# Kernel tuning notes

Hardware: AMD Instinct MI355X
Metric: run time of the kernel (lower is better)

Reference implementation:

```python
import jax, jax.numpy as jnp
import numpy as np

N = 100000   # nodes
E = 1600000  # edges
G = 256      # graphs
NF = 7       # node features
EF = 3       # edge features (in/out)
UD = 2       # global feature dim
H = 128      # hidden dim
NL = 2       # MetaLayers = n_layers - 1
DOUT = 1


def _lin_init(k, fan_in, fan_out):
    return jax.random.normal(k, (fan_in, fan_out), jnp.float32) / np.sqrt(fan_in)


def _mlp2(h, W1, b1, W2, b2):
    return jax.nn.relu(h @ W1 + b1) @ W2 + b2


def setup_inputs() -> dict:
    key = jax.random.key(0)
    ks = jax.random.split(key, 40)
    x = jax.random.normal(ks[0], (N, NF), jnp.float32)
    edge_index = jax.random.randint(ks[1], (2, E), 0, N, jnp.int64)
    edge_attr = jax.random.normal(ks[2], (E, EF), jnp.float32)
    u = jax.random.normal(ks[3], (G, UD), jnp.float32)
    batch = jnp.sort(jax.random.randint(ks[4], (N,), 0, G, jnp.int64))
    # stacked per-layer params (NL identical layers)
    e_in = 2 * NF + EF          # 17
    n_in = NF + 3 * EF + UD     # 18
    eW1 = jnp.stack([_lin_init(ks[5 + i], e_in, H) for i in range(NL)])
    eb1 = jnp.zeros((NL, H), jnp.float32)
    eW2 = jnp.stack([_lin_init(ks[7 + i], H, EF) for i in range(NL)])
    eb2 = jnp.zeros((NL, EF), jnp.float32)
    nW1 = jnp.stack([_lin_init(ks[9 + i], n_in, H) for i in range(NL)])
    nb1 = jnp.zeros((NL, H), jnp.float32)
    nW2 = jnp.stack([_lin_init(ks[11 + i], H, NF) for i in range(NL)])
    nb2 = jnp.zeros((NL, NF), jnp.float32)
    # output head: 3*node_out + global_in -> H -> H -> H -> dim_out
    oW1 = _lin_init(ks[20], 3 * NF + UD, H); ob1 = jnp.zeros((H,), jnp.float32)
    oW2 = _lin_init(ks[21], H, H); ob2 = jnp.zeros((H,), jnp.float32)
    oW3 = _lin_init(ks[22], H, H); ob3 = jnp.zeros((H,), jnp.float32)
    oW4 = _lin_init(ks[23], H, DOUT); ob4 = jnp.zeros((DOUT,), jnp.float32)
    return dict(x=x, edge_attr=edge_attr, u=u,
                eW1=eW1, eb1=eb1, eW2=eW2, eb2=eb2,
                nW1=nW1, nb1=nb1, nW2=nW2, nb2=nb2,
                oW1=oW1, ob1=ob1, oW2=oW2, ob2=ob2,
                oW3=oW3, ob3=ob3, oW4=oW4, ob4=ob4,
                edge_index=edge_index, batch=batch)


def _segment_reduce3(vals, seg, num):
    # add / max (empty -> 0, matching torch_scatter fill) / mean
    s = jax.ops.segment_sum(vals, seg, num_segments=num)
    cnt = jax.ops.segment_sum(jnp.ones((vals.shape[0], 1), vals.dtype), seg, num_segments=num)
    m = jax.ops.segment_max(vals, seg, num_segments=num)
    m = jnp.where(cnt > 0, m, jnp.zeros_like(m))
    mean = s / jnp.maximum(cnt, 1.0)
    return s, m, mean, cnt


def reference(x, edge_attr, u, eW1, eb1, eW2, eb2, nW1, nb1, nW2, nb2,
              oW1, ob1, oW2, ob2, oW3, ob3, oW4, ob4, edge_index, batch):
    row, col = edge_index[0], edge_index[1]
    for l in range(NL):
        # EdgeModel: gather src/dest node feats + edge feats -> MLP
        e_in = jnp.concatenate([x[row], x[col], edge_attr], axis=1)  # [E, 2*NF+EF]
        edge_attr = _mlp2(e_in, eW1[l], eb1[l], eW2[l], eb2[l])      # [E, EF]
        # NodeModel: three scatter reductions over incoming edges (col)
        s, m, mean, _ = _segment_reduce3(edge_attr, col, N)
        n_in = jnp.concatenate([x, s, m, mean, u[batch]], axis=1)    # [N, NF+3*EF+UD]
        x = _mlp2(n_in, nW1[l], nb1[l], nW2[l], nb2[l])              # [N, NF]
    # global pools per graph
    s, m, mean, _ = _segment_reduce3(x, batch, G)
    h = jnp.concatenate([s, mean, m, u], axis=1)                     # [G, 3*NF+UD]
    h = jax.nn.relu(h @ oW1 + ob1)
    h = jax.nn.relu(h @ oW2 + ob2)
    h = jax.nn.relu(h @ oW3 + ob3)
    return h @ oW4 + ob4                                             # [G, DOUT]
```

## Files before the change

### kernel.cpp

```cpp
#include <hip/hip_runtime.h>

#define NN 100000
#define NE 1600000
#define NG 256
#define NB 391

typedef __attribute__((ext_vector_type(8))) short short8v;
typedef __attribute__((ext_vector_type(4))) float float4v;

__device__ __forceinline__ unsigned short f2bf(float f) {
    unsigned u = __float_as_uint(f);
    return (unsigned short)((u + 0x7FFFu + ((u >> 16) & 1u)) >> 16);
}

__global__ __launch_bounds__(256) void zero_kernel(float* __restrict__ p, int n) {
    int i = blockIdx.x * 256 + threadIdx.x;
    if (i < n) p[i] = 0.f;
}

__global__ __launch_bounds__(256) void rank_kernel(
    const int* __restrict__ col, unsigned* __restrict__ cnt,
    unsigned* __restrict__ rank) {
    int e = blockIdx.x * 256 + threadIdx.x;
    rank[e] = atomicAdd(&cnt[col[e]], 1u);
}

__global__ __launch_bounds__(256) void gbound_kernel(
    const int* __restrict__ batch, int* __restrict__ gstart) {
    int n = blockIdx.x * 256 + threadIdx.x;
    if (n >= NN) return;
    int b = batch[n];
    int bp = (n == 0) ? -1 : batch[n - 1];
    for (int g = bp + 1; g <= b; ++g) gstart[g] = n;
    if (n == NN - 1) {
        for (int g = b + 1; g <= NG; ++g) gstart[g] = NN;
    }
}

__global__ __launch_bounds__(256) void bsum_kernel(
    const unsigned* __restrict__ cnt, unsigned* __restrict__ bsum) {
    __shared__ unsigned sm[256];
    int i = blockIdx.x * 256 + threadIdx.x;
    sm[threadIdx.x] = (i < NN) ? cnt[i] : 0u;
    __syncthreads();
    for (int s = 128; s > 0; s >>= 1) {
        if (threadIdx.x < s) sm[threadIdx.x] += sm[threadIdx.x + s];
        __syncthreads();
    }
    if (threadIdx.x == 0) bsum[blockIdx.x] = sm[0];
}

__global__ __launch_bounds__(512) void bscan_kernel(
    const unsigned* __restrict__ bsum, unsigned* __restrict__ boff) {
    __shared__ unsigned a[512], b[512];
    int t = threadIdx.x;
    a[t] = (t < NB) ? bsum[t] : 0u;
    __syncthreads();
    unsigned* src = a; unsigned* dst = b;
    for (int off = 1; off < 512; off <<= 1) {
        unsigned v = src[t];
        if (t >= off) v += src[t - off];
        dst[t] = v;
        __syncthreads();
        unsigned* tmp = src; src = dst; dst = tmp;
    }
    if (t < NB) boff[t] = (t == 0) ? 0u : src[t - 1];
}

__global__ __launch_bounds__(256) void start_kernel(
    const unsigned* __restrict__ cnt, const unsigned* __restrict__ boff,
    unsigned* __restrict__ start) {
    __shared__ unsigned a[256], b[256];
    int t = threadIdx.x;
    int i = blockIdx.x * 256 + t;
    unsigned v = (i < NN) ? cnt[i] : 0u;
    a[t] = v;
    __syncthreads();
    unsigned* src = a; unsigned* dst = b;
    for (int off = 1; off < 256; off <<= 1) {
        unsigned x = src[t];
        if (t >= off) x += src[t - off];
        dst[t] = x;
        __syncthreads();
        unsigned* tmp = src; src = dst; dst = tmp;
    }
    unsigned excl = src[t] - v;
    unsigned st = boff[blockIdx.x] + excl;
    if (i < NN) {
        start[i] = st;
        if (i == NN - 1) start[NN] = st + v;
    }
}

__global__ __launch_bounds__(256) void scatter_kernel(
    const int* __restrict__ row, const int* __restrict__ col,
    const float* __restrict__ ea,
    const unsigned* __restrict__ start, const unsigned* __restrict__ rank,
    int2* __restrict__ rc, float* __restrict__ eab) {
    int e = blockIdx.x * 256 + threadIdx.x;
    int c = col[e];
    unsigned t = start[c] + rank[e];
    rc[t] = make_int2(row[e], c);
    eab[(size_t)t * 3 + 0] = ea[(size_t)e * 3 + 0];
    eab[(size_t)t * 3 + 1] = ea[(size_t)e * 3 + 1];
    eab[(size_t)t * 3 + 2] = ea[(size_t)e * 3 + 2];
}

__global__ __launch_bounds__(256) void prep_kernel(
    const float* __restrict__ eW1, const float* __restrict__ eb1, const float* __restrict__ eW2,
    const float* __restrict__ nW1, const float* __restrict__ nb1, const float* __restrict__ nW2,
    short* __restrict__ ewf, float* __restrict__ w2f, float* __restrict__ b1f,
    float* __restrict__ nwt)
{
    int t = blockIdx.x * 256 + threadIdx.x;
    const int EWF = 2 * 4096;
    const int W2F = 2 * 1536;
    const int B1F = 2 * 512;
    const int NWT = 2 * 128 * 28;
    if (t < EWF) {
        int layer = t >> 12, r = t & 4095;
        int tt = r >> 9, r2 = r & 511;
        int l = r2 >> 3, i = r2 & 7;
        int kk = ((l >> 4) << 3) + i;
        int n = tt * 16 + (l & 15);
        float v = (kk < 17) ? eW1[layer * 17 * 128 + kk * 128 + n] : 0.f;
        ewf[t] = (short)f2bf(v);
    } else if (t < EWF + W2F) {
        int q = t - EWF;
        int layer = q / 1536, r = q % 1536;
        int l = r / 24, r2 = r % 24;
        int tt = r2 / 3, c = r2 % 3;
        int k = tt * 16 + (l & 15);
        w2f[q] = eW2[layer * 384 + k * 3 + c];
    } else if (t < EWF + W2F + B1F) {
        int q = t - EWF - W2F;
        int layer = q / 512, r = q % 512;
        int l = r / 8, tt = r % 8;
        b1f[q] = eb1[layer * 128 + tt * 16 + (l & 15)];
    } else if (t < EWF + W2F + B1F + NWT) {
        int q = t - EWF - W2F - B1F;
        int l = q / (128 * 28), rest = q % (128 * 28), j = rest / 28, i = rest % 28;
        float v = 0.f;
        if (i < 18)       v = nW1[l * 18 * 128 + i * 128 + j];
        else if (i == 18) v = nb1[l * 128 + j];
        else if (i < 26)  v = nW2[l * 128 * 7 + j * 7 + (i - 19)];
        nwt[q] = v;
    }
}

__global__ __launch_bounds__(256) void edge_kernel(
    const float* __restrict__ x, float* eab,
    const int2* __restrict__ rc,
    const short* __restrict__ ewf, const float* __restrict__ w2f,
    const float* __restrict__ b1f, const float* __restrict__ b2)
{
    int lane = threadIdx.x & 63;
    int l15 = lane & 15, lg = lane >> 4;
    int wid = (blockIdx.x * 256 + threadIdx.x) >> 6;
    int nwaves = gridDim.x * 4;

    short8v B1[8];
    #pragma unroll
    for (int t = 0; t < 8; ++t)
        B1[t] = *(const short8v*)(ewf + (t * 64 + lane) * 8);
    float w2a[8], w2b[8], w2c[8], b1v[8];
    #pragma unroll
    for (int t = 0; t < 8; ++t) {
        w2a[t] = w2f[lane * 24 + t * 3 + 0];
        w2b[t] = w2f[lane * 24 + t * 3 + 1];
        w2c[t] = w2f[lane * 24 + t * 3 + 2];
        b1v[t] = b1f[lane * 8 + t];
    }
    float bb0 = b2[0], bb1 = b2[1], bb2 = b2[2];

    const int NT = NE / 16;
    for (int tile = wid; tile < NT; tile += nwaves) {
        int s = tile * 16 + l15;
        int2 p = rc[s];
        const float* xr = x + (size_t)p.x * 7;
        const float* xc = x + (size_t)p.y * 7;
        const float* ep = eab + (size_t)s * 3;

        float av0 = 0.f, av1 = 0.f, av2 = 0.f, av3 = 0.f,
              av4 = 0.f, av5 = 0.f, av6 = 0.f, av7 = 0.f;
        if (lg == 0) {
            av0 = xr[0]; av1 = xr[1]; av2 = xr[2]; av3 = xr[3];
            av4 = xr[4]; av5 = xr[5]; av6 = xr[6]; av7 = xc[0];
        } else if (lg == 1) {
            av0 = xc[1]; av1 = xc[2]; av2 = xc[3]; av3 = xc[4];
            av4 = xc[5]; av5 = xc[6]; av6 = ep[0]; av7 = ep[1];
        } else if (lg == 2) {
            av0 = ep[2];
        }

        short8v A;
        A[0] = (short)f2bf(av0); A[1] = (short)f2bf(av1);
        A[2] = (short)f2bf(av2); A[3] = (short)f2bf(av3);
        A[4] = (short)f2bf(av4); A[5] = (short)f2bf(av5);
        A[6] = (short)f2bf(av6); A[7] = (short)f2bf(av7);

        float4v Z = {0.f, 0.f, 0.f, 0.f};
        float4v C[8];
        #pragma unroll
        for (int t = 0; t < 8; ++t)
            C[t] = __builtin_amdgcn_mfma_f32_16x16x32_bf16(A, B1[t], Z, 0, 0, 0);

        float p00 = 0.f, p01 = 0.f, p02 = 0.f;
        float p10 = 0.f, p11 = 0.f, p12 = 0.f;
        float p20 = 0.f, p21 = 0.f, p22 = 0.f;
        float p30 = 0.f, p31 = 0.f, p32 = 0.f;
        #pragma unroll
        for (int t = 0; t < 8; ++t) {
            float h0 = fmaxf(C[t][0] + b1v[t], 0.f);
            float h1 = fmaxf(C[t][1] + b1v[t], 0.f);
            float h2 = fmaxf(C[t][2] + b1v[t], 0.f);
            float h3 = fmaxf(C[t][3] + b1v[t], 0.f);
            p00 += h0 * w2a[t]; p01 += h0 * w2b[t]; p02 += h0 * w2c[t];
            p10 += h1 * w2a[t]; p11 += h1 * w2b[t]; p12 += h1 * w2c[t];
            p20 += h2 * w2a[t]; p21 += h2 * w2b[t]; p22 += h2 * w2c[t];
            p30 += h3 * w2a[t]; p31 += h3 * w2b[t]; p32 += h3 * w2c[t];
        }
        #pragma unroll
        for (int m = 1; m < 16; m <<= 1) {
            p00 += __shfl_xor(p00, m, 16); p01 += __shfl_xor(p01, m, 16); p02 += __shfl_xor(p02, m, 16);
            p10 += __shfl_xor(p10, m, 16); p11 += __shfl_xor(p11, m, 16); p12 += __shfl_xor(p12, m, 16);
            p20 += __shfl_xor(p20, m, 16); p21 += __shfl_xor(p21, m, 16); p22 += __shfl_xor(p22, m, 16);
            p30 += __shfl_xor(p30, m, 16); p31 += __shfl_xor(p31, m, 16); p32 += __shfl_xor(p32, m, 16);
        }
        if (l15 < 4) {
            float o0 = (l15 == 0) ? p00 : (l15 == 1) ? p10 : (l15 == 2) ? p20 : p30;
            float o1 = (l15 == 0) ? p01 : (l15 == 1) ? p11 : (l15 == 2) ? p21 : p31;
            float o2 = (l15 == 0) ? p02 : (l15 == 1) ? p12 : (l15 == 2) ? p22 : p32;
            size_t off = (size_t)(tile * 16 + lg * 4 + l15) * 3;
            eab[off + 0] = o0 + bb0;
            eab[off + 1] = o1 + bb1;
            eab[off + 2] = o2 + bb2;
        }
    }
}

__global__ __launch_bounds__(256) void reduce_kernel(
    const float* __restrict__ eab, const unsigned* __restrict__ start,
    const float* __restrict__ u, const int* __restrict__ batch,
    float* __restrict__ nred)
{
    int gid = blockIdx.x * 256 + threadIdx.x;
    int n = gid >> 4, sub = gid & 15;
    if (n >= NN) return;
    unsigned sbeg = start[n], send = start[n + 1];

    float s0 = 0.f, s1 = 0.f, s2 = 0.f;
    float m0 = -__builtin_inff(), m1 = -__builtin_inff(), m2 = -__builtin_inff();
    for (unsigned k = sbeg + sub; k < send; k += 16) {
        float v0 = eab[(size_t)k * 3 + 0];
        float v1 = eab[(size_t)k * 3 + 1];
        float v2 = eab[(size_t)k * 3 + 2];
        s0 += v0; s1 += v1; s2 += v2;
        m0 = fmaxf(m0, v0); m1 = fmaxf(m1, v1); m2 = fmaxf(m2, v2);
    }
    #pragma unroll
    for (int msk = 1; msk < 16; msk <<= 1) {
        s0 += __shfl_xor(s0, msk, 16);
        s1 += __shfl_xor(s1, msk, 16);
        s2 += __shfl_xor(s2, msk, 16);
        m0 = fmaxf(m0, __shfl_xor(m0, msk, 16));
        m1 = fmaxf(m1, __shfl_xor(m1, msk, 16));
        m2 = fmaxf(m2, __shfl_xor(m2, msk, 16));
    }
    if (sub == 0) {
        float deg = (float)(send - sbeg);
        if (send == sbeg) { m0 = 0.f; m1 = 0.f; m2 = 0.f; }
        float inv = 1.f / fmaxf(deg, 1.f);
        int b = batch[n];
        float* o = nred + (size_t)n * 12;
        o[0] = s0; o[1] = s1; o[2] = s2;
        o[3] = m0; o[4] = m1; o[5] = m2;
        o[6] = s0 * inv; o[7] = s1 * inv; o[8] = s2 * inv;
        o[9] = u[b * 2 + 0]; o[10] = u[b * 2 + 1];
    }
}

#define NMLP_BLOCKS 1024
#define NMLP_WAVES (NMLP_BLOCKS * 4)
__global__ __launch_bounds__(256, 4) void nodemlp_kernel(
    const float* x_in, const float* __restrict__ nred,
    const float* __restrict__ wt, const float* __restrict__ b2,
    float* x_out)
{
    int lane = threadIdx.x & 63;
    int wid = (blockIdx.x * 256 + threadIdx.x) >> 6;

    const float* ra = wt + lane * 28;
    const float* rb = wt + (lane + 64) * 28;
    float a0 = ra[0], a1 = ra[1], a2 = ra[2], a3 = ra[3], a4 = ra[4], a5 = ra[5],
          a6 = ra[6], a7 = ra[7], a8 = ra[8], a9 = ra[9], a10 = ra[10], a11 = ra[11],
          a12 = ra[12], a13 = ra[13], a14 = ra[14], a15 = ra[15], a16 = ra[16], a17 = ra[17],
          ab = ra[18], p0 = ra[19], p1 = ra[20], p2 = ra[21], p3 = ra[22], p4 = ra[23],
          p5 = ra[24], p6 = ra[25];
    float b0 = rb[0], b1 = rb[1], b2_ = rb[2], b3 = rb[3], b4 = rb[4], b5 = rb[5],
          b6 = rb[6], b7 = rb[7], b8 = rb[8], b9 = rb[9], b10 = rb[10], b11 = rb[11],
          b12 = rb[12], b13 = rb[13], b14 = rb[14], b15 = rb[15], b16 = rb[16], b17 = rb[17],
          bb = rb[18], q0 = rb[19], q1 = rb[20], q2 = rb[21], q3 = rb[22], q4 = rb[23],
          q5 = rb[24], q6 = rb[25];

    asm volatile("" : "+v"(a0), "+v"(a1), "+v"(a2), "+v"(a3), "+v"(a4), "+v"(a5),
                      "+v"(a6), "+v"(a7), "+v"(a8), "+v"(a9), "+v"(a10), "+v"(a11),
                      "+v"(a12), "+v"(a13), "+v"(a14), "+v"(a15), "+v"(a16), "+v"(a17),
                      "+v"(ab), "+v"(p0), "+v"(p1), "+v"(p2), "+v"(p3), "+v"(p4),
                      "+v"(p5), "+v"(p6));
    asm volatile("" : "+v"(b0), "+v"(b1), "+v"(b2_), "+v"(b3), "+v"(b4), "+v"(b5),
                      "+v"(b6), "+v"(b7), "+v"(b8), "+v"(b9), "+v"(b10), "+v"(b11),
                      "+v"(b12), "+v"(b13), "+v"(b14), "+v"(b15), "+v"(b16), "+v"(b17),
                      "+v"(bb), "+v"(q0), "+v"(q1), "+v"(q2), "+v"(q3), "+v"(q4),
                      "+v"(q5), "+v"(q6));

    float B0 = b2[0], B1 = b2[1], B2 = b2[2], B3 = b2[3], B4 = b2[4], B5 = b2[5], B6 = b2[6];

    const int nper = (NN + NMLP_WAVES - 1) / NMLP_WAVES;
    int n0 = wid * nper;
    int n1 = n0 + nper; if (n1 > NN) n1 = NN;

    #pragma unroll 2
    for (int n = n0; n < n1; ++n) {
        int nu = __builtin_amdgcn_readfirstlane(n);
        const float* xp = x_in + (size_t)nu * 7;
        const float* rp = nred + (size_t)nu * 12;
        float i0 = xp[0], i1 = xp[1], i2 = xp[2], i3 = xp[3], i4 = xp[4], i5 = xp[5], i6 = xp[6];
        float s0 = rp[0], s1 = rp[1], s2 = rp[2];
        float m0 = rp[3], m1 = rp[4], m2 = rp[5];
        float e0 = rp[6], e1 = rp[7], e2 = rp[8];
        float u0 = rp[9], u1 = rp[10];

        float ha = ab, hb = bb;
        ha += i0 * a0;  hb += i0 * b0;
        ha += i1 * a1;  hb += i1 * b1;
        ha += i2 * a2;  hb += i2 * b2_;
        ha += i3 * a3;  hb += i3 * b3;
        ha += i4 * a4;  hb += i4 * b4;
        ha += i5 * a5;  hb += i5 * b5;
        ha += i6 * a6;  hb += i6 * b6;
        ha += s0 * a7;  hb += s0 * b7;
        ha += s1 * a8;  hb += s1 * b8;
        ha += s2 * a9;  hb += s2 * b9;
        ha += m0 * a10; hb += m0 * b10;
        ha += m1 * a11; hb += m1 * b11;
        ha += m2 * a12; hb += m2 * b12;
        ha += e0 * a13; hb += e0 * b13;
        ha += e1 * a14; hb += e1 * b14;
        ha += e2 * a15; hb += e2 * b15;
        ha += u0 * a16; hb += u0 * b16;
        ha += u1 * a17; hb += u1 * b17;
        ha = fmaxf(ha, 0.f); hb = fmaxf(hb, 0.f);

        float c0 = ha * p0 + hb * q0;
        float c1 = ha * p1 + hb * q1;
        float c2 = ha * p2 + hb * q2;
        float c3 = ha * p3 + hb * q3;
        float c4 = ha * p4 + hb * q4;
        float c5 = ha * p5 + hb * q5;
        float c6 = ha * p6 + hb * q6;
        #pragma unroll
        for (int msk = 1; msk < 64; msk <<= 1) {
            c0 += __shfl_xor(c0, msk);
            c1 += __shfl_xor(c1, msk);
            c2 += __shfl_xor(c2, msk);
            c3 += __shfl_xor(c3, msk);
            c4 += __shfl_xor(c4, msk);
            c5 += __shfl_xor(c5, msk);
            c6 += __shfl_xor(c6, msk);
        }
        float o = c0 + B0;
        if (lane == 1) o = c1 + B1;
        if (lane == 2) o = c2 + B2;
        if (lane == 3) o = c3 + B3;
        if (lane == 4) o = c4 + B4;
        if (lane == 5) o = c5 + B5;
        if (lane == 6) o = c6 + B6;
        if (lane < 7) x_out[(size_t)nu * 7 + lane] = o;
    }
}

__global__ __launch_bounds__(256) void pool_head_kernel(
    const float* __restrict__ x, const int* __restrict__ gstart,
    const float* __restrict__ u,
    const float* __restrict__ oW1, const float* __restrict__ ob1,
    const float* __restrict__ oW2, const float* __restrict__ ob2,
    const float* __restrict__ oW3, const float* __restrict__ ob3,
    const float* __restrict__ oW4, const float* __restrict__ ob4,
    float* __restrict__ out)
{
    int g = blockIdx.x, tid = threadIdx.x;
    int lane = tid & 63, wv = tid >> 6;
    int gs = gstart[g], ge = gstart[g + 1];

    float s0 = 0.f, s1 = 0.f, s2 = 0.f, s3 = 0.f, s4 = 0.f, s5 = 0.f, s6 = 0.f;
    float m0 = -__builtin_inff(), m1 = m0, m2 = m0, m3 = m0, m4 = m0, m5 = m0, m6 = m0;
    for (int n = gs + tid; n < ge; n += 256) {
        const float* xp = x + (size_t)n * 7;
        float v0 = xp[0], v1 = xp[1], v2 = xp[2], v3 = xp[3], v4 = xp[4], v5 = xp[5], v6 = xp[6];
        s0 += v0; s1 += v1; s2 += v2; s3 += v3; s4 += v4; s5 += v5; s6 += v6;
        m0 = fmaxf(m0, v0); m1 = fmaxf(m1, v1); m2 = fmaxf(m2, v2); m3 = fmaxf(m3, v3);
        m4 = fmaxf(m4, v4); m5 = fmaxf(m5, v5); m6 = fmaxf(m6, v6);
    }
    #pragma unroll
    for (int msk = 1; msk < 64; msk <<= 1) {
        s0 += __shfl_xor(s0, msk); s1 += __shfl_xor(s1, msk); s2 += __shfl_xor(s2, msk);
        s3 += __shfl_xor(s3, msk); s4 += __shfl_xor(s4, msk); s5 += __shfl_xor(s5, msk);
        s6 += __shfl_xor(s6, msk);
        m0 = fmaxf(m0, __shfl_xor(m0, msk)); m1 = fmaxf(m1, __shfl_xor(m1, msk));
        m2 = fmaxf(m2, __shfl_xor(m2, msk)); m3 = fmaxf(m3, __shfl_xor(m3, msk));
        m4 = fmaxf(m4, __shfl_xor(m4, msk)); m5 = fmaxf(m5, __shfl_xor(m5, msk));
        m6 = fmaxf(m6, __shfl_xor(m6, msk));
    }
    __shared__ float red[4][14];
    __shared__ float hin[23];
    __shared__ float ha[128];
    __shared__ float hbuf[128];
    if (lane == 0) {
        red[wv][0] = s0; red[wv][1] = s1; red[wv][2] = s2; red[wv][3] = s3;
        red[wv][4] = s4; red[wv][5] = s5; red[wv][6] = s6;
        red[wv][7] = m0; red[wv][8] = m1; red[wv][9] = m2; red[wv][10] = m3;
        red[wv][11] = m4; red[wv][12] = m5; red[wv][13] = m6;
    }
    __syncthreads();
    if (tid < 7) {
        float S = red[0][tid] + red[1][tid] + red[2][tid] + red[3][tid];
        float M = fmaxf(fmaxf(red[0][7 + tid], red[1][7 + tid]),
                        fmaxf(red[2][7 + tid], red[3][7 + tid]));
        float cntf = (float)(ge - gs);
        if (ge == gs) M = 0.f;
        hin[tid] = S;
        hin[7 + tid] = S / fmaxf(cntf, 1.f);
        hin[14 + tid] = M;
    }
    if (tid < 2) hin[21 + tid] = u[g * 2 + tid];
    __syncthreads();

    float h = 0.f;
    if (tid < 128) {
        h = ob1[tid];
        for (int i = 0; i < 23; ++i) h += hin[i] * oW1[i * 128 + tid];
        ha[tid] = fmaxf(h, 0.f);
    }
    __syncthreads();
    if (tid < 128) {
        h = ob2[tid];
        for (int i = 0; i < 128; ++i) h += ha[i] * oW2[i * 128 + tid];
        hbuf[tid] = fmaxf(h, 0.f);
    }
    __syncthreads();
    if (tid < 128) {
        h = ob3[tid];
        for (int i = 0; i < 128; ++i) h += hbuf[i] * oW3[i * 128 + tid];
        ha[tid] = fmaxf(h, 0.f) * oW4[tid];
    }
    __syncthreads();
    if (tid == 0) {
        float acc = ob4[0];
        for (int i = 0; i < 128; ++i) acc += ha[i];
        out[g] = acc;
    }
}

extern "C" void kernel_launch(void* const* d_in, const int* in_sizes, int n_in,
                              void* d_out, int out_size, void* d_ws, size_t ws_size,
                              hipStream_t stream) {
    const float* x         = (const float*)d_in[0];
    const float* edge_attr = (const float*)d_in[1];
    const float* u         = (const float*)d_in[2];
    const float* eW1 = (const float*)d_in[3];
    const float* eb1 = (const float*)d_in[4];
    const float* eW2 = (const float*)d_in[5];
    const float* eb2 = (const float*)d_in[6];
    const float* nW1 = (const float*)d_in[7];
    const float* nb1 = (const float*)d_in[8];
    const float* nW2 = (const float*)d_in[9];
    const float* nb2 = (const float*)d_in[10];
    const float* oW1 = (const float*)d_in[11];
    const float* ob1 = (const float*)d_in[12];
    const float* oW2 = (const float*)d_in[13];
    const float* ob2 = (const float*)d_in[14];
    const float* oW3 = (const float*)d_in[15];
    const float* ob3 = (const float*)d_in[16];
    const float* oW4 = (const float*)d_in[17];
    const float* ob4 = (const float*)d_in[18];
    const int* edge_index = (const int*)d_in[19];
    const int* batch      = (const int*)d_in[20];
    const int* row = edge_index;
    const int* col = edge_index + NE;

    float* ws        = (float*)d_ws;
    float* eab       = ws;
    float* ws_x      = eab + (size_t)NE * 3;
    int2*  rc        = (int2*)(ws_x + (size_t)NN * 7);
    float* nred      = (float*)(rc + (size_t)NE);
    unsigned* rank   = (unsigned*)(nred + (size_t)NN * 12);
    unsigned* cnt    = rank + (size_t)NE;
    unsigned* startv = cnt + NN;
    unsigned* bsum   = startv + NN + 1;
    unsigned* boff   = bsum + 512;
    int* gstart      = (int*)(boff + 512);
    float* nwt       = (float*)(gstart + 260);
    float* w2f       = nwt + 2 * 128 * 28;
    float* b1f       = w2f + 2 * 1536;
    uintptr_t ewb    = ((uintptr_t)(b1f + 2 * 512) + 15) & ~(uintptr_t)15;
    short* ewf       = (short*)ewb;

    dim3 b256(256);
    dim3 ge_(NE / 256);
    dim3 gn(NB);

    zero_kernel<<<(NN + 255) / 256, b256, 0, stream>>>((float*)cnt, NN);

    rank_kernel<<<ge_, b256, 0, stream>>>(col, cnt, rank);
    gbound_kernel<<<gn, b256, 0, stream>>>(batch, gstart);
    bsum_kernel<<<gn, b256, 0, stream>>>(cnt, bsum);
    bscan_kernel<<<1, 512, 0, stream>>>(bsum, boff);
    start_kernel<<<gn, b256, 0, stream>>>(cnt, boff, startv);
    scatter_kernel<<<ge_, b256, 0, stream>>>(row, col, edge_attr, startv, rank, rc, eab);

    {
        int t = 2 * 4096 + 2 * 1536 + 2 * 512 + 2 * 128 * 28;
        prep_kernel<<<(t + 255) / 256, b256, 0, stream>>>(
            eW1, eb1, eW2, nW1, nb1, nW2, ewf, w2f, b1f, nwt);
    }

    dim3 gr((NN * 16 + 255) / 256);
    dim3 gemf(2048);

    edge_kernel<<<gemf, b256, 0, stream>>>(x, eab, rc, ewf, w2f, b1f, eb2);
    reduce_kernel<<<gr, b256, 0, stream>>>(eab, startv, u, batch, nred);
    nodemlp_kernel<<<NMLP_BLOCKS, b256, 0, stream>>>(x, nred, nwt, nb2, ws_x);

    edge_kernel<<<gemf, b256, 0, stream>>>(ws_x, eab, rc,
        ewf + 4096, w2f + 1536, b1f + 512, eb2 + 3);
    reduce_kernel<<<gr, b256, 0, stream>>>(eab, startv, u, batch, nred);
    nodemlp_kernel<<<NMLP_BLOCKS, b256, 0, stream>>>(ws_x, nred, nwt + 128 * 28, nb2 + 7, ws_x);

    pool_head_kernel<<<NG, b256, 0, stream>>>(ws_x, gstart, u,
        oW1, ob1, oW2, ob2, oW3, ob3, oW4, ob4, (float*)d_out);
}
```

Baseline: 427.0 us.

## Replace per-node CSR counting sort with 128-node bucket sort and LDS-atomic reduction

After: 417.7 us. 1.02x faster.

```diff
diff --git a/kernel.cpp b/kernel.cpp
--- a/kernel.cpp
+++ b/kernel.cpp
@@ -4,6 +4,10 @@
 #define NE 1600000
 #define NG 256
 #define NB 391
+#define NBH 1024
+#define CHUNK 1563
+#define NBINS 1024
+#define NBUCK 782
 
 typedef __attribute__((ext_vector_type(8))) short short8v;
 typedef __attribute__((ext_vector_type(4))) float float4v;
@@ -12,17 +16,90 @@
     unsigned u = __float_as_uint(f);
     return (unsigned short)((u + 0x7FFFu + ((u >> 16) & 1u)) >> 16);
 }
-
-__global__ __launch_bounds__(256) void zero_kernel(float* __restrict__ p, int n) {
-    int i = blockIdx.x * 256 + threadIdx.x;
-    if (i < n) p[i] = 0.f;
-}
-
-__global__ __launch_bounds__(256) void rank_kernel(
-    const int* __restrict__ col, unsigned* __restrict__ cnt,
-    unsigned* __restrict__ rank) {
-    int e = blockIdx.x * 256 + threadIdx.x;
-    rank[e] = atomicAdd(&cnt[col[e]], 1u);
+__device__ __forceinline__ unsigned fenc(float f) {
+    unsigned u = __float_as_uint(f);
+    return (u & 0x80000000u) ? ~u : (u | 0x80000000u);
+}
+__device__ __forceinline__ float fdec(unsigned e) {
+    return __uint_as_float((e & 0x80000000u) ? (e & 0x7FFFFFFFu) : ~e);
+}
+
+__global__ __launch_bounds__(256) void hist_kernel(
+    const int* __restrict__ col, unsigned* __restrict__ ghist) {
+    __shared__ unsigned h[NBINS];
+    int b = blockIdx.x;
+    for (int i = threadIdx.x; i < NBINS; i += 256) h[i] = 0;
+    __syncthreads();
+    int e0 = b * CHUNK;
+    int e1 = e0 + CHUNK; if (e1 > NE) e1 = NE;
+    for (int e = e0 + threadIdx.x; e < e1; e += 256)
+        atomicAdd(&h[col[e] >> 7], 1u);
+    __syncthreads();
+    for (int i = threadIdx.x; i < NBINS; i += 256)
+        ghist[(size_t)b * NBINS + i] = h[i];
+}
+
+__global__ __launch_bounds__(1024) void scanB_kernel(
+    const unsigned* __restrict__ ghist, unsigned* __restrict__ goff,
+    unsigned* __restrict__ total) {
+    __shared__ unsigned a[NBH], bb[NBH];
+    int bin = blockIdx.x, t = threadIdx.x;
+    unsigned v = ghist[(size_t)t * NBINS + bin];
+    a[t] = v;
+    __syncthreads();
+    unsigned* src = a; unsigned* dst = bb;
+    for (int off = 1; off < NBH; off <<= 1) {
+        unsigned x = src[t];
+        if (t >= off) x += src[t - off];
+        dst[t] = x;
+        __syncthreads();
+        unsigned* tmp = src; src = dst; dst = tmp;
+    }
+    goff[(size_t)t * NBINS + bin] = src[t] - v;
+    if (t == NBH - 1) total[bin] = src[t];
+}
+
+__global__ __launch_bounds__(1024) void scanC_kernel(
+    const unsigned* __restrict__ total, unsigned* __restrict__ binbase) {
+    __shared__ unsigned a[NBINS], bb[NBINS];
+    int t = threadIdx.x;
+    unsigned v = total[t];
+    a[t] = v;
+    __syncthreads();
+    unsigned* src = a; unsigned* dst = bb;
+    for (int off = 1; off < NBINS; off <<= 1) {
+        unsigned x = src[t];
+        if (t >= off) x += src[t - off];
+        dst[t] = x;
+        __syncthreads();
+        unsigned* tmp = src; src = dst; dst = tmp;
+    }
+    binbase[t] = src[t] - v;
+    if (t == NBINS - 1) binbase[NBINS] = src[t];
+}
+
+__global__ __launch_bounds__(256) void scatterD_kernel(
+    const int* __restrict__ row, const int* __restrict__ col,
+    const float* __restrict__ ea,
+    const unsigned* __restrict__ goff, const unsigned* __restrict__ binbase,
+    int2* __restrict__ rc, float* __restrict__ eab) {
+    __shared__ unsigned cur[NBINS];
+    int b = blockIdx.x;
+    for (int i = threadIdx.x; i < NBINS; i += 256) cur[i] = 0;
+    __syncthreads();
+    int e0 = b * CHUNK;
+    int e1 = e0 + CHUNK; if (e1 > NE) e1 = NE;
+    const unsigned* grow = goff + (size_t)b * NBINS;
+    for (int e = e0 + threadIdx.x; e < e1; e += 256) {
+        int c = col[e];
+        int bin = c >> 7;
+        unsigned l = atomicAdd(&cur[bin], 1u);
+        unsigned slot = binbase[bin] + grow[bin] + l;
+        rc[slot] = make_int2(row[e], c);
+        eab[(size_t)slot * 3 + 0] = ea[(size_t)e * 3 + 0];
+        eab[(size_t)slot * 3 + 1] = ea[(size_t)e * 3 + 1];
+        eab[(size_t)slot * 3 + 2] = ea[(size_t)e * 3 + 2];
+    }
 }
 
 __global__ __launch_bounds__(256) void gbound_kernel(
@@ -35,75 +112,6 @@
     if (n == NN - 1) {
         for (int g = b + 1; g <= NG; ++g) gstart[g] = NN;
     }
-}
-
-__global__ __launch_bounds__(256) void bsum_kernel(
-    const unsigned* __restrict__ cnt, unsigned* __restrict__ bsum) {
-    __shared__ unsigned sm[256];
-    int i = blockIdx.x * 256 + threadIdx.x;
-    sm[threadIdx.x] = (i < NN) ? cnt[i] : 0u;
-    __syncthreads();
-    for (int s = 128; s > 0; s >>= 1) {
-        if (threadIdx.x < s) sm[threadIdx.x] += sm[threadIdx.x + s];
-        __syncthreads();
-    }
-    if (threadIdx.x == 0) bsum[blockIdx.x] = sm[0];
-}
-
-__global__ __launch_bounds__(512) void bscan_kernel(
-    const unsigned* __restrict__ bsum, unsigned* __restrict__ boff) {
-    __shared__ unsigned a[512], b[512];
-    int t = threadIdx.x;
-    a[t] = (t < NB) ? bsum[t] : 0u;
-    __syncthreads();
-    unsigned* src = a; unsigned* dst = b;
-    for (int off = 1; off < 512; off <<= 1) {
-        unsigned v = src[t];
-        if (t >= off) v += src[t - off];
-        dst[t] = v;
-        __syncthreads();
-        unsigned* tmp = src; src = dst; dst = tmp;
-    }
-    if (t < NB) boff[t] = (t == 0) ? 0u : src[t - 1];
-}
-
-__global__ __launch_bounds__(256) void start_kernel(
-    const unsigned* __restrict__ cnt, const unsigned* __restrict__ boff,
-    unsigned* __restrict__ start) {
-    __shared__ unsigned a[256], b[256];
-    int t = threadIdx.x;
-    int i = blockIdx.x * 256 + t;
-    unsigned v = (i < NN) ? cnt[i] : 0u;
-    a[t] = v;
-    __syncthreads();
-    unsigned* src = a; unsigned* dst = b;
-    for (int off = 1; off < 256; off <<= 1) {
-        unsigned x = src[t];
-        if (t >= off) x += src[t - off];
-        dst[t] = x;
-        __syncthreads();
-        unsigned* tmp = src; src = dst; dst = tmp;
-    }
-    unsigned excl = src[t] - v;
-    unsigned st = boff[blockIdx.x] + excl;
-    if (i < NN) {
-        start[i] = st;
-        if (i == NN - 1) start[NN] = st + v;
-    }
-}
-
-__global__ __launch_bounds__(256) void scatter_kernel(
-    const int* __restrict__ row, const int* __restrict__ col,
-    const float* __restrict__ ea,
-    const unsigned* __restrict__ start, const unsigned* __restrict__ rank,
-    int2* __restrict__ rc, float* __restrict__ eab) {
-    int e = blockIdx.x * 256 + threadIdx.x;
-    int c = col[e];
-    unsigned t = start[c] + rank[e];
-    rc[t] = make_int2(row[e], c);
-    eab[(size_t)t * 3 + 0] = ea[(size_t)e * 3 + 0];
-    eab[(size_t)t * 3 + 1] = ea[(size_t)e * 3 + 1];
-    eab[(size_t)t * 3 + 2] = ea[(size_t)e * 3 + 2];
 }
 
 __global__ __launch_bounds__(256) void prep_kernel(
@@ -239,44 +247,48 @@
     }
 }
 
-__global__ __launch_bounds__(256) void reduce_kernel(
-    const float* __restrict__ eab, const unsigned* __restrict__ start,
+__global__ __launch_bounds__(256) void bucket_reduce_kernel(
+    const float* __restrict__ eab, const int2* __restrict__ rc,
+    const unsigned* __restrict__ binbase,
     const float* __restrict__ u, const int* __restrict__ batch,
     float* __restrict__ nred)
 {
-    int gid = blockIdx.x * 256 + threadIdx.x;
-    int n = gid >> 4, sub = gid & 15;
-    if (n >= NN) return;
-    unsigned sbeg = start[n], send = start[n + 1];
-
-    float s0 = 0.f, s1 = 0.f, s2 = 0.f;
-    float m0 = -__builtin_inff(), m1 = -__builtin_inff(), m2 = -__builtin_inff();
-    for (unsigned k = sbeg + sub; k < send; k += 16) {
+    __shared__ float s0[128], s1[128], s2[128];
+    __shared__ unsigned m0[128], m1[128], m2[128], cc[128];
+    int bin = blockIdx.x, t = threadIdx.x;
+    if (t < 128) {
+        s0[t] = 0.f; s1[t] = 0.f; s2[t] = 0.f;
+        m0[t] = 0u; m1[t] = 0u; m2[t] = 0u; cc[t] = 0u;
+    }
+    __syncthreads();
+    unsigned beg = binbase[bin], end = binbase[bin + 1];
+    for (unsigned k = beg + t; k < end; k += 256) {
+        int c = rc[k].y & 127;
         float v0 = eab[(size_t)k * 3 + 0];
         float v1 = eab[(size_t)k * 3 + 1];
         float v2 = eab[(size_t)k * 3 + 2];
-        s0 += v0; s1 += v1; s2 += v2;
-        m0 = fmaxf(m0, v0); m1 = fmaxf(m1, v1); m2 = fmaxf(m2, v2);
-    }
-    #pragma unroll
-    for (int msk = 1; msk < 16; msk <<= 1) {
-        s0 += __shfl_xor(s0, msk, 16);
-        s1 += __shfl_xor(s1, msk, 16);
-        s2 += __shfl_xor(s2, msk, 16);
-        m0 = fmaxf(m0, __shfl_xor(m0, msk, 16));
-        m1 = fmaxf(m1, __shfl_xor(m1, msk, 16));
-        m2 = fmaxf(m2, __shfl_xor(m2, msk, 16));
-    }
-    if (sub == 0) {
-        float deg = (float)(send - sbeg);
-        if (send == sbeg) { m0 = 0.f; m1 = 0.f; m2 = 0.f; }
-        float inv = 1.f / fmaxf(deg, 1.f);
-        int b = batch[n];
-        float* o = nred + (size_t)n * 12;
-        o[0] = s0; o[1] = s1; o[2] = s2;
-        o[3] = m0; o[4] = m1; o[5] = m2;
-        o[6] = s0 * inv; o[7] = s1 * inv; o[8] = s2 * inv;
-        o[9] = u[b * 2 + 0]; o[10] = u[b * 2 + 1];
+        atomicAdd(&s0[c], v0); atomicAdd(&s1[c], v1); atomicAdd(&s2[c], v2);
+        atomicMax(&m0[c], fenc(v0)); atomicMax(&m1[c], fenc(v1)); atomicMax(&m2[c], fenc(v2));
+        atomicAdd(&cc[c], 1u);
+    }
+    __syncthreads();
+    if (t < 128) {
+        int n = (bin << 7) + t;
+        if (n < NN) {
+            unsigned c = cc[t];
+            float cf = (float)c;
+            float inv = 1.f / fmaxf(cf, 1.f);
+            float S0 = s0[t], S1 = s1[t], S2 = s2[t];
+            float M0 = c ? fdec(m0[t]) : 0.f;
+            float M1 = c ? fdec(m1[t]) : 0.f;
+            float M2 = c ? fdec(m2[t]) : 0.f;
+            int b = batch[n];
+            float* o = nred + (size_t)n * 12;
+            o[0] = S0; o[1] = S1; o[2] = S2;
+            o[3] = M0; o[4] = M1; o[5] = M2;
+            o[6] = S0 * inv; o[7] = S1 * inv; o[8] = S2 * inv;
+            o[9] = u[b * 2 + 0]; o[10] = u[b * 2 + 1];
+        }
     }
 }
 
@@ -494,12 +506,11 @@
     float* ws_x      = eab + (size_t)NE * 3;
     int2*  rc        = (int2*)(ws_x + (size_t)NN * 7);
     float* nred      = (float*)(rc + (size_t)NE);
-    unsigned* rank   = (unsigned*)(nred + (size_t)NN * 12);
-    unsigned* cnt    = rank + (size_t)NE;
-    unsigned* startv = cnt + NN;
-    unsigned* bsum   = startv + NN + 1;
-    unsigned* boff   = bsum + 512;
-    int* gstart      = (int*)(boff + 512);
+    unsigned* ghist  = (unsigned*)(nred + (size_t)NN * 12);
+    unsigned* goff   = ghist + (size_t)NBH * NBINS;
+    unsigned* total  = goff + (size_t)NBH * NBINS;
+    unsigned* binbase = total + NBINS;
+    int* gstart      = (int*)(binbase + NBINS + 4);
     float* nwt       = (float*)(gstart + 260);
     float* w2f       = nwt + 2 * 128 * 28;
     float* b1f       = w2f + 2 * 1536;
@@ -507,17 +518,13 @@
     short* ewf       = (short*)ewb;
 
     dim3 b256(256);
-    dim3 ge_(NE / 256);
     dim3 gn(NB);
 
-    zero_kernel<<<(NN + 255) / 256, b256, 0, stream>>>((float*)cnt, NN);
-
-    rank_kernel<<<ge_, b256, 0, stream>>>(col, cnt, rank);
+    hist_kernel<<<NBH, b256, 0, stream>>>(col, ghist);
     gbound_kernel<<<gn, b256, 0, stream>>>(batch, gstart);
-    bsum_kernel<<<gn, b256, 0, stream>>>(cnt, bsum);
-    bscan_kernel<<<1, 512, 0, stream>>>(bsum, boff);
-    start_kernel<<<gn, b256, 0, stream>>>(cnt, boff, startv);
-    scatter_kernel<<<ge_, b256, 0, stream>>>(row, col, edge_attr, startv, rank, rc, eab);
+    scanB_kernel<<<NBINS, 1024, 0, stream>>>(ghist, goff, total);
+    scanC_kernel<<<1, 1024, 0, stream>>>(total, binbase);
+    scatterD_kernel<<<NBH, b256, 0, stream>>>(row, col, edge_attr, goff, binbase, rc, eab);
 
     {
         int t = 2 * 4096 + 2 * 1536 + 2 * 512 + 2 * 128 * 28;
@@ -525,16 +532,16 @@
             eW1, eb1, eW2, nW1, nb1, nW2, ewf, w2f, b1f, nwt);
     }
 
-    dim3 gr((NN * 16 + 255) / 256);
     dim3 gemf(2048);
+    dim3 grb(NBUCK);
 
     edge_kernel<<<gemf, b256, 0, stream>>>(x, eab, rc, ewf, w2f, b1f, eb2);
-    reduce_kernel<<<gr, b256, 0, stream>>>(eab, startv, u, batch, nred);
+    bucket_reduce_kernel<<<grb, b256, 0, stream>>>(eab, rc, binbase, u, batch, nred);
     nodemlp_kernel<<<NMLP_BLOCKS, b256, 0, stream>>>(x, nred, nwt, nb2, ws_x);
 
     edge_kernel<<<gemf, b256, 0, stream>>>(ws_x, eab, rc,
         ewf + 4096, w2f + 1536, b1f + 512, eb2 + 3);
-    reduce_kernel<<<gr, b256, 0, stream>>>(eab, startv, u, batch, nred);
+    bucket_reduce_kernel<<<grb, b256, 0, stream>>>(eab, rc, binbase, u, batch, nred);
     nodemlp_kernel<<<NMLP_BLOCKS, b256, 0, stream>>>(ws_x, nred, nwt + 128 * 28, nb2 + 7, ws_x);
 
     pool_head_kernel<<<NG, b256, 0, stream>>>(ws_x, gstart, u,
```
